# Performance work log

Measured on AMD Instinct MI355X. Metric: run time of the kernel, lower is better.

Reference implementation:

```python
import jax, jax.numpy as jnp
import numpy as np

B, S, H = 2, 1024, 1024
NH, HD = 8, 128
E, TOPK, MI = 8, 2, 1024
SI = 2 * MI  # shared experts intermediate (n_shared_experts=2)
EPS = 1e-6
THETA = 10000.0


def setup_inputs() -> dict:
    key = jax.random.key(0)
    ks = jax.random.split(key, 16)
    w = lambda k, shp: (0.02 * jax.random.normal(k, shp, dtype=jnp.float32))
    # RoPE tables [S, HD]
    inv_freq = 1.0 / (THETA ** (np.arange(0, HD, 2, dtype=np.float32) / HD))
    t = np.arange(S, dtype=np.float32)
    freqs = np.outer(t, inv_freq)
    emb = np.concatenate([freqs, freqs], axis=-1)
    return {
        "hidden_states": jax.random.normal(ks[0], (B, S, H), dtype=jnp.float32),
        "ln1_w": jnp.ones((H,), jnp.float32),
        "ln2_w": jnp.ones((H,), jnp.float32),
        "q_w": w(ks[1], (H, H)),
        "k_w": w(ks[2], (H, H)),
        "v_w": w(ks[3], (H, H)),
        "o_w": w(ks[4], (H, H)),
        "cos": jnp.asarray(np.cos(emb), jnp.float32),
        "sin": jnp.asarray(np.sin(emb), jnp.float32),
        "gate_w": w(ks[5], (E, H)),
        "eg_w": w(ks[6], (E, MI, H)),
        "eu_w": w(ks[7], (E, MI, H)),
        "ed_w": w(ks[8], (E, H, MI)),
        "sg_w": w(ks[9], (SI, H)),
        "su_w": w(ks[10], (SI, H)),
        "sd_w": w(ks[11], (H, SI)),
    }


def _rmsnorm(x, w):
    return x * jax.lax.rsqrt(jnp.mean(x * x, axis=-1, keepdims=True) + EPS) * w


def _rotate_half(x):
    x1, x2 = jnp.split(x, 2, axis=-1)
    return jnp.concatenate([-x2, x1], axis=-1)


def _attention(x, q_w, k_w, v_w, o_w, cos, sin):
    b, s, h = x.shape
    q = (x @ q_w.T).reshape(b, s, NH, HD)
    k = (x @ k_w.T).reshape(b, s, NH, HD)
    v = (x @ v_w.T).reshape(b, s, NH, HD)
    c = cos[None, :s, None, :]
    sn = sin[None, :s, None, :]
    q = q * c + _rotate_half(q) * sn
    k = k * c + _rotate_half(k) * sn
    scores = jnp.einsum("bqhd,bkhd->bhqk", q, k) / jnp.sqrt(jnp.float32(HD))
    causal = jnp.tril(jnp.ones((s, s), dtype=bool))
    scores = jnp.where(causal[None, None], scores, -jnp.inf)
    p = jax.nn.softmax(scores, axis=-1)
    out = jnp.einsum("bhqk,bkhd->bqhd", p, v).reshape(b, s, h)
    return out @ o_w.T


def _mlp(x, gw, uw, dw):
    return (jax.nn.silu(x @ gw.T) * (x @ uw.T)) @ dw.T


def _moe(x, gate_w, eg_w, eu_w, ed_w, sg_w, su_w, sd_w):
    b, s, h = x.shape
    xt = x.reshape(-1, h)                              # [T, H]
    T = xt.shape[0]
    probs = jax.nn.softmax(xt @ gate_w.T, axis=-1)     # [T, E]
    rw, idx = jax.lax.top_k(probs, TOPK)               # [T, K]
    rw = rw / (jnp.sum(rw, axis=-1, keepdims=True) + 1e-20)  # norm_topk_prob
    # dense combine weights [T, E] (zero for unselected experts)
    w_full = jnp.zeros((T, E), xt.dtype).at[jnp.arange(T)[:, None], idx].add(rw)
    # dense all-expert compute, masked-combined (faithful to per-token loop math)
    g = jax.nn.silu(jnp.einsum("th,eih->tei", xt, eg_w))
    u = jnp.einsum("th,eih->tei", xt, eu_w)
    y = jnp.einsum("tei,ehi->teh", g * u, ed_w)        # [T, E, H]
    routed = jnp.einsum("teh,te->th", y, w_full)
    shared = _mlp(xt, sg_w, su_w, sd_w)
    return (routed + shared).reshape(b, s, h)


def reference(hidden_states, ln1_w, ln2_w, q_w, k_w, v_w, o_w, cos, sin,
              gate_w, eg_w, eu_w, ed_w, sg_w, su_w, sd_w):
    x = hidden_states
    x = x + _attention(_rmsnorm(x, ln1_w), q_w, k_w, v_w, o_w, cos, sin)
    x = x + _moe(_rmsnorm(x, ln2_w), gate_w, eg_w, eu_w, ed_w, sg_w, su_w, sd_w)
    return x
```

## Files before the change

kernel.cpp:

```cpp
#include <hip/hip_runtime.h>

#define B_   2
#define S_   1024
#define H_   1024
#define NH_  8
#define HD_  128
#define E_   8
#define MI_  1024
#define SI_  2048
#define T_   2048
#define CAP_ 2048

typedef unsigned short u16;
typedef __attribute__((ext_vector_type(4))) float f32x4;
typedef __attribute__((ext_vector_type(4))) unsigned short u16x4;
typedef __attribute__((ext_vector_type(8))) unsigned short u16x8;
typedef __attribute__((ext_vector_type(8))) __bf16 bf16x8;

__device__ __forceinline__ u16 f2bf(float f) {
  unsigned int u = __builtin_bit_cast(unsigned int, f);
  u = (u + 0x7fffu + ((u >> 16) & 1u)) >> 16;
  return (u16)u;
}
__device__ __forceinline__ float bf2f(u16 u) {
  return __builtin_bit_cast(float, (unsigned int)u << 16);
}
__device__ __forceinline__ float wave_sum(float v) {
#pragma unroll
  for (int o = 32; o; o >>= 1) v += __shfl_down(v, o, 64);
  return v;
}
__device__ __forceinline__ void gll16(const u16* g, u16* l) {
  __builtin_amdgcn_global_load_lds((const __attribute__((address_space(1))) void*)g,
                                   (__attribute__((address_space(3))) void*)l, 16, 0, 0);
}

__global__ void cvt_all(const float* __restrict__ q_w, const float* __restrict__ k_w,
                        const float* __restrict__ v_w, const float* __restrict__ o_w,
                        const float* __restrict__ eg_w, const float* __restrict__ eu_w,
                        const float* __restrict__ ed_w, const float* __restrict__ sg_w,
                        const float* __restrict__ su_w, const float* __restrict__ sd_w,
                        u16* __restrict__ qwb, u16* __restrict__ egu, u16* __restrict__ edb,
                        u16* __restrict__ sgu, u16* __restrict__ sdb) {
  int tid = threadIdx.x;
  const float* src[8];
  u16* dst[8];
#pragma unroll
  for (int g = 0; g < 8; g++) {
    int row = blockIdx.x * 8 + g;
    if (row < 4096) {
      int seg = row >> 10;
      const float* in = (seg == 0) ? q_w : (seg == 1) ? k_w : (seg == 2) ? v_w : o_w;
      src[g] = in + (long)(row & 1023) * 1024;
      dst[g] = qwb + (long)row * 1024;
    } else if (row < 20480) {
      int rel = row - 4096;
      int zu = rel >= 8192;
      int r = rel & 8191;
      int e = r >> 10, i = r & 1023;
      int orow = (i >> 4) * 32 + (i & 15) + (zu ? 16 : 0);
      src[g] = (zu ? eu_w : eg_w) + (long)r * 1024;
      dst[g] = egu + ((long)e * 2048 + orow) * 1024;
    } else if (row < 28672) {
      long f = (long)(row - 20480) * 1024;
      src[g] = ed_w + f;
      dst[g] = edb + f;
    } else if (row < 32768) {
      int rel = row - 28672;
      int zu = rel >= 2048;
      int i = rel & 2047;
      int orow = (i >> 4) * 32 + (i & 15) + (zu ? 16 : 0);
      src[g] = (zu ? su_w : sg_w) + (long)i * 1024;
      dst[g] = sgu + (long)orow * 1024;
    } else {
      long f = (long)(row - 32768) * 1024;
      src[g] = sd_w + f;
      dst[g] = sdb + f;
    }
  }
  f32x4 v[8];
#pragma unroll
  for (int g = 0; g < 8; g++)
    v[g] = __builtin_nontemporal_load((const f32x4*)src[g] + tid);
#pragma unroll
  for (int g = 0; g < 8; g++) {
    u16x4 o;
#pragma unroll
    for (int c = 0; c < 4; c++) o[c] = f2bf(v[g][c]);
    ((u16x4*)dst[g])[tid] = o;
  }
}

__global__ void rmsnorm_cvt(const float* __restrict__ x, const float* __restrict__ w,
                            u16* __restrict__ out) {
  int t = blockIdx.x, tid = threadIdx.x;
  f32x4 v = ((const f32x4*)(x + (long)t * H_))[tid];
  float ss = v[0]*v[0] + v[1]*v[1] + v[2]*v[2] + v[3]*v[3];
  __shared__ float red[4];
  float s = wave_sum(ss);
  if ((tid & 63) == 0) red[tid >> 6] = s;
  __syncthreads();
  float r = rsqrtf((red[0] + red[1] + red[2] + red[3]) * (1.0f / H_) + 1e-6f);
  f32x4 wv = ((const f32x4*)w)[tid];
  u16x4 o;
#pragma unroll
  for (int c = 0; c < 4; c++) o[c] = f2bf(v[c] * r * wv[c]);
  ((u16x4*)(out + (long)t * H_))[tid] = o;
}

__global__ void rmsnorm2_gate(const float* __restrict__ x1, const float* __restrict__ ln2w,
                              const float* __restrict__ gw, u16* __restrict__ xn,
                              int* __restrict__ eidx, float* __restrict__ aw) {
  int t = blockIdx.x, tid = threadIdx.x;
  int lane = tid & 63, wave = tid >> 6;
  f32x4 v = ((const f32x4*)(x1 + (long)t * H_))[tid];
  float ss = v[0]*v[0] + v[1]*v[1] + v[2]*v[2] + v[3]*v[3];
  __shared__ float redS[4];
  __shared__ float redE[4][E_];
  float s = wave_sum(ss);
  if (lane == 0) redS[wave] = s;
  __syncthreads();
  float r = rsqrtf((redS[0] + redS[1] + redS[2] + redS[3]) * (1.0f / H_) + 1e-6f);
  f32x4 wv = ((const f32x4*)ln2w)[tid];
  float xv[4];
  u16x4 o;
#pragma unroll
  for (int c = 0; c < 4; c++) { xv[c] = v[c] * r * wv[c]; o[c] = f2bf(xv[c]); }
  ((u16x4*)(xn + (long)t * H_))[tid] = o;
  float acc[E_];
#pragma unroll
  for (int e = 0; e < E_; e++) {
    f32x4 g = ((const f32x4*)(gw + (long)e * H_))[tid];
    acc[e] = xv[0]*g[0] + xv[1]*g[1] + xv[2]*g[2] + xv[3]*g[3];
  }
#pragma unroll
  for (int e = 0; e < E_; e++) acc[e] = wave_sum(acc[e]);
  if (lane == 0)
#pragma unroll
    for (int e = 0; e < E_; e++) redE[wave][e] = acc[e];
  __syncthreads();
  if (tid == 0) {
    float l[E_];
#pragma unroll
    for (int e = 0; e < E_; e++) l[e] = redE[0][e] + redE[1][e] + redE[2][e] + redE[3][e];
    float mx = l[0];
#pragma unroll
    for (int e = 1; e < E_; e++) mx = fmaxf(mx, l[e]);
    float p[E_], z = 0.f;
#pragma unroll
    for (int e = 0; e < E_; e++) { p[e] = __expf(l[e] - mx); z += p[e]; }
    int e0 = 0;
#pragma unroll
    for (int e = 1; e < E_; e++) if (p[e] > p[e0]) e0 = e;
    int e1 = (e0 == 0) ? 1 : 0;
#pragma unroll
    for (int e = 0; e < E_; e++) if (e != e0 && p[e] > p[e1]) e1 = e;
    float q0 = p[e0] / z, q1 = p[e1] / z;
    float invs = 1.0f / (q0 + q1 + 1e-20f);
    eidx[t * 2] = e0;
    eidx[t * 2 + 1] = e1;
    aw[t * 2] = q0 * invs;
    aw[t * 2 + 1] = q1 * invs;
  }
}

__global__ __launch_bounds__(256) void route_scan(const int* __restrict__ eidx,
                                                  int* __restrict__ arow,
                                                  int* __restrict__ cursor,
                                                  int* __restrict__ itok) {
  __shared__ int sc[E_][256];
  int tid = threadIdx.x;
  unsigned c0 = 0, c1 = 0;
  int ebuf[16];
#pragma unroll
  for (int i = 0; i < 16; i++) {
    int e = eidx[tid * 16 + i];
    ebuf[i] = e;
    if (e < 4) c0 += 1u << (8 * e); else c1 += 1u << (8 * (e - 4));
  }
#pragma unroll
  for (int e = 0; e < E_; e++)
    sc[e][tid] = (e < 4) ? (int)((c0 >> (8 * e)) & 0xff) : (int)((c1 >> (8 * (e - 4))) & 0xff);
  __syncthreads();
  for (int st = 1; st < 256; st <<= 1) {
    int v[E_];
#pragma unroll
    for (int e = 0; e < E_; e++) v[e] = (tid >= st) ? sc[e][tid - st] : 0;
    __syncthreads();
#pragma unroll
    for (int e = 0; e < E_; e++) sc[e][tid] += v[e];
    __syncthreads();
  }
  if (tid == 255)
#pragma unroll
    for (int e = 0; e < E_; e++) cursor[e] = sc[e][255];
  int base[E_];
#pragma unroll
  for (int e = 0; e < E_; e++) {
    int own = (e < 4) ? (int)((c0 >> (8 * e)) & 0xff) : (int)((c1 >> (8 * (e - 4))) & 0xff);
    base[e] = sc[e][tid] - own;
  }
  __syncthreads();
#pragma unroll
  for (int e = 0; e < E_; e++) sc[e][tid] = base[e];
  __syncthreads();
  unsigned r0 = 0, r1 = 0;
#pragma unroll
  for (int i = 0; i < 16; i++) {
    int e = ebuf[i];
    int run = (e < 4) ? (int)((r0 >> (8 * e)) & 0xff) : (int)((r1 >> (8 * (e - 4))) & 0xff);
    int row = e * CAP_ + sc[e][tid] + run;
    arow[tid * 16 + i] = row;
    itok[row] = (tid * 16 + i) >> 1;
    if (e < 4) r0 += 1u << (8 * e); else r1 += 1u << (8 * (e - 4));
  }
}

__global__ void rope_cvt(const u16* __restrict__ qf, const float* __restrict__ cs,
                         const float* __restrict__ sn, u16* __restrict__ qbb) {
  const u16* q = qf + (long)blockIdx.z * 2097152;
  u16* qb = qbb + (long)blockIdx.z * 2097152;
  int rid = blockIdx.x * 2 + (threadIdx.x >> 7);
  int d = threadIdx.x & 127;
  int h = rid & (NH_ - 1);
  int bs = rid >> 3;
  int s = bs & (S_ - 1);
  int b = bs >> 10;
  long base = (long)rid * HD_;
  float v = bf2f(q[base + d]);
  float o = (d < 64) ? (-bf2f(q[base + d + 64])) : bf2f(q[base + d - 64]);
  float res = v * cs[s * HD_ + d] + o * sn[s * HD_ + d];
  qb[((long)((b * NH_ + h) * S_ + s)) * HD_ + d] = f2bf(res);
}

__global__ void vtrans(const u16* __restrict__ v, u16* __restrict__ vt) {
  int bh = blockIdx.z, b = bh >> 3, h = bh & 7;
  int s0 = blockIdx.x * 32, d0 = blockIdx.y * 32;
  __shared__ u16 tile[32][33];
  for (int i = threadIdx.y; i < 32; i += 8) {
    tile[i][threadIdx.x] = v[(((long)(b * S_ + s0 + i)) * NH_ + h) * HD_ + d0 + threadIdx.x];
  }
  __syncthreads();
  for (int i = threadIdx.y; i < 32; i += 8) {
    vt[((long)bh * HD_ + d0 + i) * S_ + s0 + threadIdx.x] = tile[threadIdx.x][i];
  }
}

__global__ __launch_bounds__(256) void flash_part(
    const u16* __restrict__ qb, const u16* __restrict__ kb,
    const u16* __restrict__ vt, u16* __restrict__ Po,
    float* __restrict__ Pm, float* __restrict__ Pl) {
  int item = blockIdx.x;
  int bh = blockIdx.y;
  int qt, ch;
  if (item < 4)       { qt = item;                    ch = 0; }
  else if (item < 12) { qt = 4 + ((item - 4) >> 1);   ch = (item - 4) & 1; }
  else if (item < 24) { qt = 8 + (item - 12) / 3;     ch = (item - 12) % 3; }
  else                { qt = 12 + ((item - 24) >> 2); ch = (item - 24) & 3; }
  int j0 = ch * 4, j1 = min(j0 + 4, qt + 1);

  int tid = threadIdx.x;
  int wavei = tid >> 6, lane = tid & 63;
  int la = lane & 15, qd = lane >> 4;

  __shared__ __align__(16) u16 Ks[64 * 128];
  __shared__ __align__(16) u16 Vs[128 * 64];
  __shared__ __align__(16) u16 Ps[4][16 * 64];

  bf16x8 qf[4];
  const u16* qrow = qb + ((long)bh * S_ + qt * 64 + wavei * 16 + la) * HD_;
#pragma unroll
  for (int ks = 0; ks < 4; ks++)
    qf[ks] = *(const bf16x8*)(qrow + ks * 32 + qd * 8);

  f32x4 oacc[8];
#pragma unroll
  for (int nf = 0; nf < 8; nf++) oacc[nf] = (f32x4){0.f, 0.f, 0.f, 0.f};
  float m_i[4], l_i[4];
#pragma unroll
  for (int r = 0; r < 4; r++) { m_i[r] = -1e30f; l_i[r] = 0.f; }

  const u16* Kbase = kb + (long)bh * S_ * HD_;
  const u16* Vbase = vt + (long)bh * HD_ * S_;
  const float scale = 0.08838834764831845f;
  u16* pw = (u16*)Ps[wavei];
  int swz = la & 7;

  for (int j = j0; j < j1; j++) {
    __syncthreads();
#pragma unroll
    for (int t = 0; t < 4; t++) {
      int blk = t * 4 + wavei;
      int kr = blk * 4 + (lane >> 4);
      int kc = (lane & 15) ^ (kr & 7);
      gll16(Kbase + ((long)j * 64 + kr) * 128 + kc * 8, Ks + blk * 512);
      int vr = blk * 8 + (lane >> 3);
      int vc = (lane & 7) ^ (vr & 7);
      gll16(Vbase + (long)vr * 1024 + j * 64 + vc * 8, Vs + blk * 512);
    }
    __syncthreads();

    f32x4 sacc[4];
#pragma unroll
    for (int jf = 0; jf < 4; jf++) sacc[jf] = (f32x4){0.f, 0.f, 0.f, 0.f};
#pragma unroll
    for (int ks = 0; ks < 4; ks++)
#pragma unroll
      for (int jf = 0; jf < 4; jf++) {
        bf16x8 kfrag = *(const bf16x8*)(Ks + (jf * 16 + la) * 128 + ((ks * 4 + qd) ^ swz) * 8);
        sacc[jf] = __builtin_amdgcn_mfma_f32_16x16x32_bf16(qf[ks], kfrag, sacc[jf], 0, 0, 0);
      }

    float sv[4][4];
    int qglob = qt * 64 + wavei * 16 + qd * 4;
#pragma unroll
    for (int jf = 0; jf < 4; jf++) {
      int kglob = j * 64 + jf * 16 + la;
#pragma unroll
      for (int r = 0; r < 4; r++)
        sv[jf][r] = (kglob <= qglob + r) ? sacc[jf][r] * scale : -1e30f;
    }
    float mnew[4], alpha[4];
#pragma unroll
    for (int r = 0; r < 4; r++) {
      float mx = fmaxf(fmaxf(sv[0][r], sv[1][r]), fmaxf(sv[2][r], sv[3][r]));
#pragma unroll
      for (int o = 1; o < 16; o <<= 1) mx = fmaxf(mx, __shfl_xor(mx, o, 64));
      mnew[r] = fmaxf(m_i[r], mx);
      alpha[r] = __expf(m_i[r] - mnew[r]);
      m_i[r] = mnew[r];
    }
#pragma unroll
    for (int r = 0; r < 4; r++) {
      float sum = 0.f;
#pragma unroll
      for (int jf = 0; jf < 4; jf++) {
        float p = __expf(sv[jf][r] - mnew[r]);
        sv[jf][r] = p;
        sum += p;
      }
#pragma unroll
      for (int o = 1; o < 16; o <<= 1) sum += __shfl_xor(sum, o, 64);
      l_i[r] = l_i[r] * alpha[r] + sum;
    }
#pragma unroll
    for (int jf = 0; jf < 4; jf++)
#pragma unroll
      for (int r = 0; r < 4; r++) {
        int rp = qd * 4 + r;
        int e = jf * 16 + la;
        pw[rp * 64 + (((e >> 3) ^ (rp & 7)) << 3) + (e & 7)] = f2bf(sv[jf][r]);
      }
#pragma unroll
    for (int nf = 0; nf < 8; nf++)
#pragma unroll
      for (int r = 0; r < 4; r++) oacc[nf][r] *= alpha[r];
#pragma unroll
    for (int ks = 0; ks < 2; ks++) {
      bf16x8 pfrag = *(const bf16x8*)(pw + la * 64 + ((ks * 4 + qd) ^ swz) * 8);
#pragma unroll
      for (int nf = 0; nf < 8; nf++) {
        bf16x8 vfrag = *(const bf16x8*)(Vs + (nf * 16 + la) * 64 + (((ks * 4 + qd) & 7) ^ swz) * 8);
        oacc[nf] = __builtin_amdgcn_mfma_f32_16x16x32_bf16(pfrag, vfrag, oacc[nf], 0, 0, 0);
      }
    }
  }

  int pidx = (bh * 16 + qt) * 4 + ch;
  int rowb = wavei * 16 + qd * 4;
  u16* pob = Po + ((long)pidx * 64 + rowb) * 128;
#pragma unroll
  for (int r = 0; r < 4; r++)
#pragma unroll
    for (int nf = 0; nf < 8; nf++)
      pob[(long)r * 128 + nf * 16 + la] = f2bf(oacc[nf][r]);
  if (la == 0)
#pragma unroll
    for (int r = 0; r < 4; r++) {
      Pm[pidx * 64 + rowb + r] = m_i[r];
      Pl[pidx * 64 + rowb + r] = l_i[r];
    }
}

__global__ __launch_bounds__(256) void attn_merge(
    const u16* __restrict__ Po, const float* __restrict__ Pm,
    const float* __restrict__ Pl, u16* __restrict__ attn) {
  int qt = blockIdx.x, bh = blockIdx.y;
  int b = bh >> 3, h = bh & 7;
  int nch = (qt >> 2) + 1;
  int t = threadIdx.x;
  int row = t >> 2, cg = (t & 3) * 32;
  long base = (long)(bh * 16 + qt) * 4;
  float mv[4], wv[4];
  float M = -1e30f;
  for (int c = 0; c < nch; c++) { mv[c] = Pm[(base + c) * 64 + row]; M = fmaxf(M, mv[c]); }
  float L = 0.f;
  for (int c = 0; c < nch; c++) { wv[c] = __expf(mv[c] - M); L += wv[c] * Pl[(base + c) * 64 + row]; }
  float inv = 1.0f / L;
  f32x4 o[8];
#pragma unroll
  for (int k = 0; k < 8; k++) o[k] = (f32x4){0.f, 0.f, 0.f, 0.f};
  for (int c = 0; c < nch; c++) {
    const u16x4* src = (const u16x4*)(Po + ((base + c) * 64 + row) * 128 + cg);
#pragma unroll
    for (int k = 0; k < 8; k++) {
      u16x4 sv = src[k];
#pragma unroll
      for (int e = 0; e < 4; e++) o[k][e] += bf2f(sv[e]) * wv[c];
    }
  }
  u16* dst = attn + ((long)b * S_ + qt * 64 + row) * H_ + h * HD_ + cg;
#pragma unroll
  for (int k = 0; k < 8; k++) {
    u16x4 ov;
#pragma unroll
    for (int c = 0; c < 4; c++) ov[c] = f2bf(o[k][c] * inv);
    ((u16x4*)dst)[k] = ov;
  }
}

__global__ void final_combine(const float* __restrict__ x1, const float* __restrict__ ys,
                              const u16* __restrict__ y, const int* __restrict__ arow,
                              const float* __restrict__ aw, float* __restrict__ out) {
  int t = blockIdx.x;
  int i = threadIdx.x * 4;
  int r0 = arow[t * 2], r1 = arow[t * 2 + 1];
  float w0 = aw[t * 2], w1 = aw[t * 2 + 1];
  f32x4 a = *(const f32x4*)(x1 + (long)t * H_ + i);
  f32x4 b = *(const f32x4*)(ys + (long)t * H_ + i);
  u16x4 y0 = *(const u16x4*)(y + (long)r0 * H_ + i);
  u16x4 y1 = *(const u16x4*)(y + (long)r1 * H_ + i);
  f32x4 o;
#pragma unroll
  for (int c = 0; c < 4; c++)
    o[c] = a[c] + b[c] + w0 * bf2f(y0[c]) + w1 * bf2f(y1[c]);
  *(f32x4*)(out + (long)t * H_ + i) = o;
}

template <int MT, int STORE_BF16, int ADD_RES, int FUSE_SILU, int IND>
__global__ __launch_bounds__(256) void gemm_bt(
    const u16* __restrict__ Ag, const u16* __restrict__ Bg, void* __restrict__ Cg,
    const float* __restrict__ Res, int K, int lda, int ldb, int ldc,
    long sAz, long sBz, long sCz, const int* __restrict__ mlimit,
    const int* __restrict__ itok) {
  constexpr int MR = MT / 32;
  int z = blockIdx.z;
  int m0 = blockIdx.y * MT, n0 = blockIdx.x * 128;
  if (mlimit && m0 >= mlimit[z]) return;
  const u16* A = Ag + (IND ? 0 : z * sAz);
  const u16* B = Bg + z * sBz;
  long cbase = (long)z * sCz;

  __shared__ __align__(16) u16 As[MT * 64];
  __shared__ __align__(16) u16 Bs[128 * 64];
  int tid = threadIdx.x;
  int lane = tid & 63, wave = tid >> 6;
  int wm = (wave & 1) * (MT / 2), wn = (wave >> 1) * 64;
  int la = lane & 15, qd = lane >> 4;
  int sr = lane >> 3;
  int scs = (lane & 7) ^ (sr & 7);

  const u16* ap[MT / 32];
  const u16* bp[4];
#pragma unroll
  for (int t = 0; t < MT / 32; t++) {
    int rloc = m0 + t * 32 + wave * 8 + sr;
    long arow_g = IND ? (long)itok[(long)z * CAP_ + rloc] : (long)rloc;
    ap[t] = A + arow_g * lda + scs * 8;
  }
#pragma unroll
  for (int t = 0; t < 4; t++)
    bp[t] = B + (long)(n0 + t * 32 + wave * 8 + sr) * ldb + scs * 8;

  f32x4 acc[MR][4];
#pragma unroll
  for (int i = 0; i < MR; i++)
#pragma unroll
    for (int j = 0; j < 4; j++) acc[i][j] = (f32x4){0.f, 0.f, 0.f, 0.f};

  int sw = la & 7;
  for (int k0 = 0; k0 < K; k0 += 64) {
    __syncthreads();
#pragma unroll
    for (int t = 0; t < MT / 32; t++)
      gll16(ap[t] + k0, As + (t * 32 + wave * 8) * 64);
#pragma unroll
    for (int t = 0; t < 4; t++)
      gll16(bp[t] + k0, Bs + (t * 32 + wave * 8) * 64);
    __syncthreads();
#pragma unroll
    for (int kk = 0; kk < 2; kk++) {
      bf16x8 af[MR], bf[4];
#pragma unroll
      for (int i = 0; i < MR; i++)
        af[i] = *(const bf16x8*)(As + (wm + i * 16 + la) * 64 + (((kk * 4 + qd) ^ sw) << 3));
#pragma unroll
      for (int j = 0; j < 4; j++)
        bf[j] = *(const bf16x8*)(Bs + (wn + j * 16 + la) * 64 + (((kk * 4 + qd) ^ sw) << 3));
#pragma unroll
      for (int i = 0; i < MR; i++)
#pragma unroll
        for (int j = 0; j < 4; j++)
          acc[i][j] = __builtin_amdgcn_mfma_f32_16x16x32_bf16(af[i], bf[j], acc[i][j], 0, 0, 0);
    }
  }

  if (FUSE_SILU) {
#pragma unroll
    for (int i = 0; i < MR; i++) {
#pragma unroll
      for (int jp = 0; jp < 2; jp++) {
        int hcol = ((n0 + wn) >> 1) + (jp << 4) + la;
#pragma unroll
        for (int r = 0; r < 4; r++) {
          int row = m0 + wm + i * 16 + qd * 4 + r;
          float g = acc[i][jp * 2][r], u = acc[i][jp * 2 + 1][r];
          float sg = g / (1.f + __expf(-g));
          ((u16*)Cg)[cbase + (long)row * ldc + hcol] = f2bf(sg * u);
        }
      }
    }
  } else {
#pragma unroll
    for (int i = 0; i < MR; i++) {
#pragma unroll
      for (int j = 0; j < 4; j++) {
        int col = n0 + wn + j * 16 + la;
#pragma unroll
        for (int r = 0; r < 4; r++) {
          int row = m0 + wm + i * 16 + qd * 4 + r;
          float v = acc[i][j][r];
          long ci = cbase + (long)row * ldc + col;
          if (ADD_RES) v += Res[(long)row * ldc + col];
          if (STORE_BF16) ((u16*)Cg)[ci] = f2bf(v);
          else ((float*)Cg)[ci] = v;
        }
      }
    }
  }
}

extern "C" void kernel_launch(void* const* d_in, const int* in_sizes, int n_in,
                              void* d_out, int out_size, void* d_ws, size_t ws_size,
                              hipStream_t stream) {
  const float* hidden = (const float*)d_in[0];
  const float* ln1w = (const float*)d_in[1];
  const float* ln2w = (const float*)d_in[2];
  const float* q_w = (const float*)d_in[3];
  const float* k_w = (const float*)d_in[4];
  const float* v_w = (const float*)d_in[5];
  const float* o_w = (const float*)d_in[6];
  const float* cosp = (const float*)d_in[7];
  const float* sinp = (const float*)d_in[8];
  const float* gate_w = (const float*)d_in[9];
  const float* eg_w = (const float*)d_in[10];
  const float* eu_w = (const float*)d_in[11];
  const float* ed_w = (const float*)d_in[12];
  const float* sg_w = (const float*)d_in[13];
  const float* su_w = (const float*)d_in[14];
  const float* sd_w = (const float*)d_in[15];
  float* out = (float*)d_out;

  char* w = (char*)d_ws;
  const size_t MB = 1u << 20;
  u16* qwb = (u16*)(w + 0 * MB);
  u16* egu = (u16*)(w + 8 * MB);
  u16* edb = (u16*)(w + 40 * MB);
  u16* sgu = (u16*)(w + 56 * MB);
  u16* sdb = (u16*)(w + 64 * MB);
  float* x1 = (float*)(w + 68 * MB);
  u16* xn = (u16*)(w + 76 * MB);
  u16* attn = (u16*)(w + 80 * MB);
  int* cursor = (int*)(w + 84 * MB);
  int* arow = (int*)(w + 84 * MB + 1024);
  float* aw = (float*)(w + 84 * MB + 20 * 1024);
  int* eidx = (int*)(w + 84 * MB + 40 * 1024);
  int* itok = (int*)(w + 84 * MB + 60 * 1024);
  u16* qkvb = (u16*)(w + 85 * MB);
  u16* qb = (u16*)(w + 109 * MB);
  u16* kb = (u16*)(w + 113 * MB);
  u16* vt = (u16*)(w + 117 * MB);
  u16* Po = (u16*)(w + 121 * MB);
  float* Pm = (float*)(w + 155 * MB);
  float* Pl = (float*)(w + 156 * MB);
  u16* hbuf = (u16*)(w + 121 * MB);
  u16* y = (u16*)(w + 157 * MB);
  u16* hs = (u16*)(w + 189 * MB);
  float* ys = (float*)(w + 197 * MB);

  const long M1 = 1048576, M2 = 2097152;

  cvt_all<<<4352, 256, 0, stream>>>(q_w, k_w, v_w, o_w, eg_w, eu_w, ed_w,
                                    sg_w, su_w, sd_w, qwb, egu, edb, sgu, sdb);

  rmsnorm_cvt<<<T_, 256, 0, stream>>>(hidden, ln1w, xn);
  gemm_bt<128, 1, 0, 0, 0><<<dim3(8, 16, 3), 256, 0, stream>>>(
      xn, qwb, qkvb, nullptr, 1024, 1024, 1024, 1024, 0, M1, M2, nullptr, nullptr);
  rope_cvt<<<dim3(8192, 1, 2), 256, 0, stream>>>(qkvb, cosp, sinp, qb);
  vtrans<<<dim3(32, 4, 16), dim3(32, 8), 0, stream>>>(qkvb + 2 * M2, vt);
  flash_part<<<dim3(40, 16), 256, 0, stream>>>(qb, kb, vt, Po, Pm, Pl);
  attn_merge<<<dim3(16, 16), 256, 0, stream>>>(Po, Pm, Pl, attn);
  gemm_bt<64, 0, 1, 0, 0><<<dim3(8, 32, 1), 256, 0, stream>>>(
      attn, qwb + 3 * M1, x1, hidden, 1024, 1024, 1024, 1024, 0, 0, 0, nullptr, nullptr);

  rmsnorm2_gate<<<T_, 256, 0, stream>>>(x1, ln2w, gate_w, xn, eidx, aw);
  hipMemsetAsync(itok, 0, E_ * CAP_ * 4, stream);
  route_scan<<<1, 256, 0, stream>>>(eidx, arow, cursor, itok);
  gemm_bt<128, 1, 0, 1, 1><<<dim3(16, 16, 8), 256, 0, stream>>>(
      xn, egu, hbuf, nullptr, 1024, 1024, 1024, MI_,
      0, (long)2 * MI_ * H_, (long)CAP_ * MI_, cursor, itok);
  gemm_bt<128, 1, 0, 0, 0><<<dim3(8, 16, 8), 256, 0, stream>>>(
      hbuf, edb, y, nullptr, 1024, 1024, 1024, 1024,
      (long)CAP_ * MI_, (long)H_ * MI_, (long)CAP_ * H_, cursor, nullptr);
  gemm_bt<128, 1, 0, 1, 0><<<dim3(32, 16, 1), 256, 0, stream>>>(
      xn, sgu, hs, nullptr, 1024, 1024, 1024, SI_, 0, 0, 0, nullptr, nullptr);
  gemm_bt<64, 0, 0, 0, 0><<<dim3(8, 32, 1), 256, 0, stream>>>(
      hs, sdb, ys, nullptr, 2048, 2048, 2048, 1024, 0, 0, 0, nullptr, nullptr);

  final_combine<<<T_, 256, 0, stream>>>(x1, ys, y, arow, aw, out);
}
```

Before: 407.9 us.

## Double-buffer GEMM LDS tiles, fuse rope with V transpose, fold rmsnorm into cvt

The GEMM now double-buffers its A/B LDS tiles, issuing the next K-tile's global-to-LDS loads before computing on the current one, with explicit vmcnt waits. This hides load latency at the cost of twice the LDS, which may lower occupancy. The RoPE and V-transpose kernels are merged into one vectorized launch, and the first rmsnorm is folded into extra blocks of the weight-conversion kernel to cut launches.

```diff
diff --git a/kernel.cpp b/kernel.cpp
--- a/kernel.cpp
+++ b/kernel.cpp
@@ -41,13 +41,31 @@
                         const float* __restrict__ ed_w, const float* __restrict__ sg_w,
                         const float* __restrict__ su_w, const float* __restrict__ sd_w,
                         u16* __restrict__ qwb, u16* __restrict__ egu, u16* __restrict__ edb,
-                        u16* __restrict__ sgu, u16* __restrict__ sdb) {
-  int tid = threadIdx.x;
+                        u16* __restrict__ sgu, u16* __restrict__ sdb,
+                        const float* __restrict__ hidden, const float* __restrict__ ln1w,
+                        u16* __restrict__ xn) {
+  int bid = blockIdx.x, tid = threadIdx.x;
+  if (bid >= 4352) {
+    int t = bid - 4352;
+    f32x4 v = ((const f32x4*)(hidden + (long)t * H_))[tid];
+    float ss = v[0]*v[0] + v[1]*v[1] + v[2]*v[2] + v[3]*v[3];
+    __shared__ float red[4];
+    float s = wave_sum(ss);
+    if ((tid & 63) == 0) red[tid >> 6] = s;
+    __syncthreads();
+    float r = rsqrtf((red[0] + red[1] + red[2] + red[3]) * (1.0f / H_) + 1e-6f);
+    f32x4 wv = ((const f32x4*)ln1w)[tid];
+    u16x4 o;
+#pragma unroll
+    for (int c = 0; c < 4; c++) o[c] = f2bf(v[c] * r * wv[c]);
+    ((u16x4*)(xn + (long)t * H_))[tid] = o;
+    return;
+  }
   const float* src[8];
   u16* dst[8];
 #pragma unroll
   for (int g = 0; g < 8; g++) {
-    int row = blockIdx.x * 8 + g;
+    int row = bid * 8 + g;
     if (row < 4096) {
       int seg = row >> 10;
       const float* in = (seg == 0) ? q_w : (seg == 1) ? k_w : (seg == 2) ? v_w : o_w;
@@ -91,23 +109,6 @@
   }
 }
 
-__global__ void rmsnorm_cvt(const float* __restrict__ x, const float* __restrict__ w,
-                            u16* __restrict__ out) {
-  int t = blockIdx.x, tid = threadIdx.x;
-  f32x4 v = ((const f32x4*)(x + (long)t * H_))[tid];
-  float ss = v[0]*v[0] + v[1]*v[1] + v[2]*v[2] + v[3]*v[3];
-  __shared__ float red[4];
-  float s = wave_sum(ss);
-  if ((tid & 63) == 0) red[tid >> 6] = s;
-  __syncthreads();
-  float r = rsqrtf((red[0] + red[1] + red[2] + red[3]) * (1.0f / H_) + 1e-6f);
-  f32x4 wv = ((const f32x4*)w)[tid];
-  u16x4 o;
-#pragma unroll
-  for (int c = 0; c < 4; c++) o[c] = f2bf(v[c] * r * wv[c]);
-  ((u16x4*)(out + (long)t * H_))[tid] = o;
-}
-
 __global__ void rmsnorm2_gate(const float* __restrict__ x1, const float* __restrict__ ln2w,
                               const float* __restrict__ gw, u16* __restrict__ xn,
                               int* __restrict__ eidx, float* __restrict__ aw) {
@@ -216,33 +217,58 @@
   }
 }
 
-__global__ void rope_cvt(const u16* __restrict__ qf, const float* __restrict__ cs,
-                         const float* __restrict__ sn, u16* __restrict__ qbb) {
-  const u16* q = qf + (long)blockIdx.z * 2097152;
-  u16* qb = qbb + (long)blockIdx.z * 2097152;
-  int rid = blockIdx.x * 2 + (threadIdx.x >> 7);
-  int d = threadIdx.x & 127;
-  int h = rid & (NH_ - 1);
-  int bs = rid >> 3;
-  int s = bs & (S_ - 1);
-  int b = bs >> 10;
-  long base = (long)rid * HD_;
-  float v = bf2f(q[base + d]);
-  float o = (d < 64) ? (-bf2f(q[base + d + 64])) : bf2f(q[base + d - 64]);
-  float res = v * cs[s * HD_ + d] + o * sn[s * HD_ + d];
-  qb[((long)((b * NH_ + h) * S_ + s)) * HD_ + d] = f2bf(res);
-}
-
-__global__ void vtrans(const u16* __restrict__ v, u16* __restrict__ vt) {
-  int bh = blockIdx.z, b = bh >> 3, h = bh & 7;
-  int s0 = blockIdx.x * 32, d0 = blockIdx.y * 32;
-  __shared__ u16 tile[32][33];
-  for (int i = threadIdx.y; i < 32; i += 8) {
-    tile[i][threadIdx.x] = v[(((long)(b * S_ + s0 + i)) * NH_ + h) * HD_ + d0 + threadIdx.x];
-  }
-  __syncthreads();
-  for (int i = threadIdx.y; i < 32; i += 8) {
-    vt[((long)bh * HD_ + d0 + i) * S_ + s0 + threadIdx.x] = tile[threadIdx.x][i];
+__global__ void rope_vtrans(const u16* __restrict__ qkvb, const float* __restrict__ cs,
+                            const float* __restrict__ sn, u16* __restrict__ qb,
+                            u16* __restrict__ kb, u16* __restrict__ vt) {
+  int bid = blockIdx.x, tid = threadIdx.x;
+  if (bid < 1024) {
+    int z = bid >> 9;
+    const u16* src = qkvb + (long)z * 2097152;
+    u16* dstb = z ? kb : qb;
+    int rb = (bid & 511) * 32 + (tid >> 3);
+    int u = tid & 7;
+    int h = rb & 7, bs = rb >> 3, s = bs & 1023, b = bs >> 10;
+    const u16* row = src + (long)rb * 128;
+    int d0 = u * 8;
+    u16x8 v1 = *(const u16x8*)(row + d0);
+    u16x8 v2 = *(const u16x8*)(row + d0 + 64);
+    const float* c1 = cs + s * 128 + d0;
+    const float* s1 = sn + s * 128 + d0;
+    u16x8 o1, o2;
+#pragma unroll
+    for (int c = 0; c < 8; c++) {
+      float a = bf2f(v1[c]), q2 = bf2f(v2[c]);
+      o1[c] = f2bf(a * c1[c] - q2 * s1[c]);
+      o2[c] = f2bf(q2 * c1[c + 64] + a * s1[c + 64]);
+    }
+    u16* orow = dstb + ((long)((b * NH_ + h) * S_ + s)) * HD_;
+    *(u16x8*)(orow + d0) = o1;
+    *(u16x8*)(orow + d0 + 64) = o2;
+  } else {
+    int vb = bid - 1024;
+    int bh = vb >> 5;
+    int rem = vb & 31;
+    int s0 = (rem >> 1) * 64, d0 = (rem & 1) * 64;
+    int b = bh >> 3, h = bh & 7;
+    __shared__ u16 tile[64][68];
+    const u16* vsrc = qkvb + 2 * 2097152;
+#pragma unroll
+    for (int it = 0; it < 4; it++) {
+      int idx = it * 256 + tid;
+      int r = idx >> 4, c = (idx & 15) * 4;
+      u16x4 vv = *(const u16x4*)(vsrc + (((long)(b * S_ + s0 + r)) * NH_ + h) * HD_ + d0 + c);
+      *(u16x4*)&tile[r][c] = vv;
+    }
+    __syncthreads();
+#pragma unroll
+    for (int it = 0; it < 4; it++) {
+      int idx = it * 256 + tid;
+      int dr = idx >> 4, sc = (idx & 15) * 4;
+      u16x4 ov;
+#pragma unroll
+      for (int k = 0; k < 4; k++) ov[k] = tile[sc + k][dr];
+      *(u16x4*)(vt + ((long)bh * HD_ + d0 + dr) * S_ + s0 + sc) = ov;
+    }
   }
 }
 
@@ -451,8 +477,8 @@
   const u16* B = Bg + z * sBz;
   long cbase = (long)z * sCz;
 
-  __shared__ __align__(16) u16 As[MT * 64];
-  __shared__ __align__(16) u16 Bs[128 * 64];
+  __shared__ __align__(16) u16 As[2][MT * 64];
+  __shared__ __align__(16) u16 Bs[2][128 * 64];
   int tid = threadIdx.x;
   int lane = tid & 63, wave = tid >> 6;
   int wm = (wave & 1) * (MT / 2), wn = (wave >> 1) * 64;
@@ -478,31 +504,47 @@
 #pragma unroll
     for (int j = 0; j < 4; j++) acc[i][j] = (f32x4){0.f, 0.f, 0.f, 0.f};
 
+  auto stage = [&](int buf, int k0) {
+#pragma unroll
+    for (int t = 0; t < MT / 32; t++)
+      gll16(ap[t] + k0, &As[buf][(t * 32 + wave * 8) * 64]);
+#pragma unroll
+    for (int t = 0; t < 4; t++)
+      gll16(bp[t] + k0, &Bs[buf][(t * 32 + wave * 8) * 64]);
+  };
+
   int sw = la & 7;
-  for (int k0 = 0; k0 < K; k0 += 64) {
-    __syncthreads();
-#pragma unroll
-    for (int t = 0; t < MT / 32; t++)
-      gll16(ap[t] + k0, As + (t * 32 + wave * 8) * 64);
-#pragma unroll
-    for (int t = 0; t < 4; t++)
-      gll16(bp[t] + k0, Bs + (t * 32 + wave * 8) * 64);
-    __syncthreads();
+  int nt = K >> 6;
+  int cur = 0;
+  stage(0, 0);
+  for (int t = 0; t < nt; ++t) {
+    if (t + 1 < nt) {
+      stage(cur ^ 1, (t + 1) * 64);
+      if constexpr (MT == 128)
+        asm volatile("s_waitcnt vmcnt(8)" ::: "memory");
+      else
+        asm volatile("s_waitcnt vmcnt(6)" ::: "memory");
+    } else {
+      asm volatile("s_waitcnt vmcnt(0)" ::: "memory");
+    }
+    __builtin_amdgcn_s_barrier();
 #pragma unroll
     for (int kk = 0; kk < 2; kk++) {
-      bf16x8 af[MR], bf[4];
+      bf16x8 af[MR], bfv[4];
 #pragma unroll
       for (int i = 0; i < MR; i++)
-        af[i] = *(const bf16x8*)(As + (wm + i * 16 + la) * 64 + (((kk * 4 + qd) ^ sw) << 3));
+        af[i] = *(const bf16x8*)(&As[cur][0] + (wm + i * 16 + la) * 64 + (((kk * 4 + qd) ^ sw) << 3));
 #pragma unroll
       for (int j = 0; j < 4; j++)
-        bf[j] = *(const bf16x8*)(Bs + (wn + j * 16 + la) * 64 + (((kk * 4 + qd) ^ sw) << 3));
+        bfv[j] = *(const bf16x8*)(&Bs[cur][0] + (wn + j * 16 + la) * 64 + (((kk * 4 + qd) ^ sw) << 3));
 #pragma unroll
       for (int i = 0; i < MR; i++)
 #pragma unroll
         for (int j = 0; j < 4; j++)
-          acc[i][j] = __builtin_amdgcn_mfma_f32_16x16x32_bf16(af[i], bf[j], acc[i][j], 0, 0, 0);
-    }
+          acc[i][j] = __builtin_amdgcn_mfma_f32_16x16x32_bf16(af[i], bfv[j], acc[i][j], 0, 0, 0);
+    }
+    __builtin_amdgcn_s_barrier();
+    cur ^= 1;
   }
 
   if (FUSE_SILU) {
@@ -590,14 +632,13 @@
 
   const long M1 = 1048576, M2 = 2097152;
 
-  cvt_all<<<4352, 256, 0, stream>>>(q_w, k_w, v_w, o_w, eg_w, eu_w, ed_w,
-                                    sg_w, su_w, sd_w, qwb, egu, edb, sgu, sdb);
-
-  rmsnorm_cvt<<<T_, 256, 0, stream>>>(hidden, ln1w, xn);
+  cvt_all<<<6400, 256, 0, stream>>>(q_w, k_w, v_w, o_w, eg_w, eu_w, ed_w,
+                                    sg_w, su_w, sd_w, qwb, egu, edb, sgu, sdb,
+                                    hidden, ln1w, xn);
+
   gemm_bt<128, 1, 0, 0, 0><<<dim3(8, 16, 3), 256, 0, stream>>>(
       xn, qwb, qkvb, nullptr, 1024, 1024, 1024, 1024, 0, M1, M2, nullptr, nullptr);
-  rope_cvt<<<dim3(8192, 1, 2), 256, 0, stream>>>(qkvb, cosp, sinp, qb);
-  vtrans<<<dim3(32, 4, 16), dim3(32, 8), 0, stream>>>(qkvb + 2 * M2, vt);
+  rope_vtrans<<<1536, 256, 0, stream>>>(qkvb, cosp, sinp, qb, kb, vt);
   flash_part<<<dim3(40, 16), 256, 0, stream>>>(qb, kb, vt, Po, Pm, Pl);
   attn_merge<<<dim3(16, 16), 256, 0, stream>>>(Po, Pm, Pl, attn);
   gemm_bt<64, 0, 1, 0, 0><<<dim3(8, 32, 1), 256, 0, stream>>>(
```

After: 389.9 us. 1.05x faster.
